# Optimization experiments

Hardware: AMD Instinct MI355X
Metric: run time of the kernel (lower is better)

Reference implementation:

```python
import jax, jax.numpy as jnp
import numpy as np
import math

H_HEADS = 4
SQRT_2_PI = math.sqrt(2.0 / math.pi)


def _gelu_tanh(x):
    return 0.5 * x * (1.0 + jnp.tanh(SQRT_2_PI * (x + 0.044715 * x ** 3)))


def _ln(x, g, b, eps=1e-5):
    mu = jnp.mean(x, axis=-1, keepdims=True)
    var = jnp.var(x, axis=-1, keepdims=True)
    return g * (x - mu) * jax.lax.rsqrt(var + eps) + b


def _forward(support_emb_mat, query_t, support_t, cls_embed, t_freq, t_phase,
             Wq, bq, Wk, bk, Wv, bv, Wo, bo, ln1_g, ln1_b, time_w,
             W1, b1, W2, b2, ln2_g, ln2_b, Wc, bc, bn_g, bn_b):
    B, F, MD = support_emb_mat.shape
    Q = query_t.shape[1]
    S = F + 1
    H = H_HEADS
    D = MD * H
    dph = D // H
    L = Wq.shape[0]
    BQ = B * Q

    # [CLS] + support sequence, feature-tiled to model_dim*num_heads
    cls = jnp.broadcast_to(cls_embed, (B, 1, MD))
    seq = jnp.concatenate([cls, support_emb_mat], axis=1)          # [B,S,MD]
    x = jnp.tile(seq, (1, 1, H))                                    # [B,S,D]
    x = jnp.broadcast_to(x[:, None], (B, Q, S, D)).reshape(BQ, S, D)

    # time sequence: [query_t_q, support_t...] per (b,q)
    sup = jnp.broadcast_to(support_t[:, None, :], (B, Q, F))
    t_seq = jnp.concatenate([query_t[..., None], sup], axis=-1).reshape(BQ, S)
    t_diff = t_seq[:, :, None] - t_seq[:, None, :]                  # [BQ,S,S]
    # time encoder: cos(t*freq + phase) -> [BQ,S,S,TD]
    t_emb = jnp.cos(t_diff[..., None] * t_freq + t_phase)

    # scale as in source: (dim_per_head // num_heads) ** -0.5
    scale = (dph // H) ** (-0.5)

    for l in range(L):
        bias = t_emb @ time_w[l]                                    # [BQ,S,S]
        add = jnp.tile(bias, (H, 1, 1))                             # [BQ*H,S,S]
        res = x
        # raw row-major reshape to (BQ*H, S, dph) exactly as torch .view
        q = (x @ Wq[l] + bq[l]).reshape(BQ * H, S, dph)
        k = (x @ Wk[l] + bk[l]).reshape(BQ * H, S, dph)
        v = (x @ Wv[l] + bv[l]).reshape(BQ * H, S, dph)
        attn = jax.nn.softmax(jnp.einsum('bsd,btd->bst', q, k) * scale + add, axis=-1)
        ctx = jnp.einsum('bst,btd->bsd', attn, v).reshape(BQ, S, D)
        out = _ln(res + ctx @ Wo[l] + bo[l], ln1_g[l], ln1_b[l])
        ffn = _gelu_tanh(out @ W1[l] + b1[l]) @ W2[l] + b2[l]
        x = _ln(out + ffn, ln2_g[l], ln2_b[l])

    # compress: Linear -> BatchNorm1d over seq channels (train mode) -> LeakyReLU
    h = x @ Wc + bc                                                 # [BQ,S,MD]
    mu = jnp.mean(h, axis=(0, 2), keepdims=True)
    var = jnp.var(h, axis=(0, 2), keepdims=True)
    h = bn_g[None, :, None] * (h - mu) * jax.lax.rsqrt(var + 1e-5) + bn_b[None, :, None]
    h = jnp.where(h >= 0, h, 0.01 * h)                              # LeakyReLU
    return h[:, 0, :].reshape(B, Q, MD)


def setup_inputs() -> dict:
    key = jax.random.key(0)
    ks = jax.random.split(key, 24)
    B, Q, F, MD = 128, 32, 7, 128
    H, L, FFN, TD = 4, 6, 2048, 32
    S = F + 1
    D = MD * H

    def nrm(k, shape, s=0.02):
        return jax.random.normal(k, shape, jnp.float32) * s

    inp = {
        'support_emb_mat': jax.random.normal(ks[0], (B, F, MD), jnp.float32),
        'query_t': jax.random.uniform(ks[1], (B, Q), jnp.float32) * 100.0,
        'support_t': jax.random.uniform(ks[2], (B, F), jnp.float32) * 100.0,
        'cls_embed': jax.random.uniform(ks[3], (1, MD), jnp.float32),
        't_freq': nrm(ks[4], (TD,), 1.0),
        't_phase': nrm(ks[5], (TD,), 1.0),
        'Wq': nrm(ks[6], (L, D, D)), 'bq': jnp.zeros((L, D)),
        'Wk': nrm(ks[7], (L, D, D)), 'bk': jnp.zeros((L, D)),
        'Wv': nrm(ks[8], (L, D, D)), 'bv': jnp.zeros((L, D)),
        'Wo': nrm(ks[9], (L, D, D)), 'bo': jnp.zeros((L, D)),
        'ln1_g': jnp.ones((L, D)), 'ln1_b': jnp.zeros((L, D)),
        'time_w': jnp.ones((L, TD)) * 0.001,
        'W1': nrm(ks[10], (L, D, FFN)), 'b1': jnp.zeros((L, FFN)),
        'W2': nrm(ks[11], (L, FFN, D)), 'b2': jnp.zeros((L, D)),
        'ln2_g': jnp.ones((L, D)), 'ln2_b': jnp.zeros((L, D)),
        'Wc': nrm(ks[12], (D, MD)), 'bc': jnp.zeros((MD,)),
        'bn_g': jnp.ones((S,)), 'bn_b': jnp.zeros((S,)),
    }
    return inp


def reference(support_emb_mat, query_t, support_t, cls_embed, t_freq, t_phase,
              Wq, bq, Wk, bk, Wv, bv, Wo, bo, ln1_g, ln1_b, time_w,
              W1, b1, W2, b2, ln2_g, ln2_b, Wc, bc, bn_g, bn_b):
    return _forward(support_emb_mat, query_t, support_t, cls_embed, t_freq, t_phase,
                    Wq, bq, Wk, bk, Wv, bv, Wo, bo, ln1_g, ln1_b, time_w,
                    W1, b1, W2, b2, ln2_g, ln2_b, Wc, bc, bn_g, bn_b)
```

## Files before the change

kernel.cpp:

```cpp
#include <hip/hip_runtime.h>
#include <hip/hip_bf16.h>

typedef _Float16 f16;
typedef __attribute__((ext_vector_type(8))) _Float16 f16x8;
typedef __attribute__((ext_vector_type(4))) _Float16 f16x4;
typedef __attribute__((ext_vector_type(4))) float f32x4;

#define DEVI __device__ __forceinline__

DEVI float ldf(const void* p, size_t i, int isf32) {
    if (isf32) return ((const float*)p)[i];
    unsigned int u = ((const unsigned short*)p)[i];
    union { unsigned int b; float f; } c; c.b = u << 16;
    return c.f;
}

DEVI void gld_lds16(const f16* g, f16* l) {
    __builtin_amdgcn_global_load_lds(
        (__attribute__((address_space(1))) void*)(g),
        (__attribute__((address_space(3))) void*)(l), 16, 0, 0);
}

__global__ void detect_dtype(const void* qt, int* flag) {
    if (threadIdx.x == 0 && blockIdx.x == 0) {
        const unsigned int* w = (const unsigned int*)qt;
        int cnt = 0;
        for (int i = 0; i < 64; ++i) {
            unsigned int lo = w[i] & 0xFFFFu;
            union { unsigned int b; float f; } c; c.b = lo << 16;
            if (c.f >= 1e-4f && c.f <= 100.5f) ++cnt;
        }
        *flag = (cnt >= 32) ? 0 : 1;
    }
}

__global__ __launch_bounds__(256)
void cvt_in(const void* __restrict__ src, float* __restrict__ dst, int n,
            const int* __restrict__ flag) {
    const int f32 = *flag;
    int i = blockIdx.x * 256 + threadIdx.x;
    if (i < n) dst[i] = ldf(src, i, f32);
}

__global__ __launch_bounds__(256)
void fill_out(float* out, float v) {
    out[blockIdx.x * 256 + threadIdx.x] = v;
}

template<int EPI>
__global__ __launch_bounds__(256, 4)
void gemm_bt(const f16* __restrict__ Ag, const f16* __restrict__ BTg,
             const float* __restrict__ biasg, const f16* __restrict__ resg,
             void* __restrict__ outg,
             int NT, int NTZ, int MCHUNK, int N, int K, int lda,
             long zsB, long zsBias, long zsC)
{
    const int tid  = threadIdx.x;
    const int w    = tid >> 6, lane = tid & 63;
    const int wm   = w >> 1,   wn   = w & 1;

    const int id    = blockIdx.x;
    const int pc    = MCHUNK * NTZ;
    const int chunk = id / pc;
    const int rem   = id - chunk * pc;
    const int mloc  = rem % MCHUNK;
    const int ynz   = rem / MCHUNK;
    const int z     = ynz / NT;
    const int tm    = (chunk * MCHUNK + mloc) * 128;
    const int tn    = (ynz - z * NT) * 128;

    const f16*   BT   = BTg + (size_t)z * zsB;
    const float* bias = biasg + (size_t)z * zsBias;
    const size_t zoffC = (size_t)z * zsC;

    __shared__ __align__(16) f16 smA[16][64][8];
    __shared__ __align__(16) f16 smB[16][64][8];

    f32x4 acc[4][4];
#pragma unroll
    for (int i = 0; i < 4; ++i)
#pragma unroll
        for (int j = 0; j < 4; ++j) acc[i][j] = (f32x4)0.0f;

    const int r16 = lane & 15, q4 = lane >> 4;
    const f16* ga[4]; const f16* gb[4];
#pragma unroll
    for (int it = 0; it < 4; ++it) {
        int sb = w * 4 + it, mt = sb >> 1, ks = sb & 1;
        ga[it] = Ag + (size_t)(tm + mt * 16 + r16) * lda + ks * 32 + q4 * 8;
        gb[it] = BT + (size_t)(tn + mt * 16 + r16) * K   + ks * 32 + q4 * 8;
    }

    const int iters = K >> 6;
    for (int kt = 0; kt < iters; ++kt) {
#pragma unroll
        for (int it = 0; it < 4; ++it) {
            int sb = w * 4 + it;
            gld_lds16(ga[it], &smA[sb][0][0]);
            gld_lds16(gb[it], &smB[sb][0][0]);
            ga[it] += 64; gb[it] += 64;
        }
        __syncthreads();
#pragma unroll
        for (int ks = 0; ks < 2; ++ks) {
            f16x8 af[4], bf[4];
#pragma unroll
            for (int i = 0; i < 4; ++i) {
                af[i] = *(const f16x8*)&smA[(wm * 4 + i) * 2 + ks][lane][0];
                bf[i] = *(const f16x8*)&smB[(wn * 4 + i) * 2 + ks][lane][0];
            }
#pragma unroll
            for (int i = 0; i < 4; ++i)
#pragma unroll
                for (int j = 0; j < 4; ++j)
                    acc[i][j] = __builtin_amdgcn_mfma_f32_16x16x32_f16(
                        af[i], bf[j], acc[i][j], 0, 0, 0);
        }
        __syncthreads();
    }

    const int rowBase = tm + wm * 64;
    const int colBase = tn + wn * 64;
#pragma unroll
    for (int j = 0; j < 4; ++j) {
        const int col = colBase + j * 16 + r16;
        const float bv = bias[col];
#pragma unroll
        for (int i = 0; i < 4; ++i) {
            const int row0 = rowBase + i * 16 + q4 * 4;
#pragma unroll
            for (int r = 0; r < 4; ++r) {
                const int row = row0 + r;
                const size_t off = (size_t)row * N + col;
                float v = acc[i][j][r] + bv;
                if constexpr (EPI == 0) {
                    ((f16*)outg)[zoffC + off] = (f16)v;
                } else if constexpr (EPI == 1) {
                    v += (float)resg[off];
                    ((f16*)outg)[off] = (f16)v;
                } else if constexpr (EPI == 2) {
                    float t  = v + 0.044715f * v * v * v;
                    float u  = 1.5957691216057308f * t;
                    float e  = __expf(u);
                    float th = 1.0f - 2.0f / (e + 1.0f);
                    ((f16*)outg)[off] = (f16)(0.5f * v * (1.0f + th));
                } else {
                    ((float*)outg)[off] = v;
                }
            }
        }
    }
}

__global__ __launch_bounds__(256)
void attn_kernel(const f16* __restrict__ qg, const f16* __restrict__ kg,
                 const f16* __restrict__ vg, const float* __restrict__ biasL,
                 f16* __restrict__ cg, int small)
{
    const int w = threadIdx.x >> 6, lane = threadIdx.x & 63;
    const int j = blockIdx.x * 4 + w;
    __shared__ __align__(16) f16 sQ[4][8][136];
    __shared__ __align__(16) f16 sK[4][8][136];
    __shared__ __align__(16) f16 sV[4][8][136];
    __shared__ float sP[4][8][8];

    const size_t base  = (size_t)j * 1024;
    const size_t ibase = small ? ((size_t)(j >> 7) * 4096 + (size_t)(j & 3) * 1024)
                               : base;
#pragma unroll
    for (int t = 0; t < 2; ++t) {
        int flat = (t * 64 + lane) * 8;
        int r = flat >> 7, c = flat & 127;
        *(f16x8*)&sQ[w][r][c] = *(const f16x8*)(qg + ibase + flat);
        *(f16x8*)&sK[w][r][c] = *(const f16x8*)(kg + ibase + flat);
        *(f16x8*)&sV[w][r][c] = *(const f16x8*)(vg + ibase + flat);
    }
    __syncthreads();

    const int i = lane >> 3, jj = lane & 7;
    float d = 0.f;
#pragma unroll
    for (int c = 0; c < 16; ++c) {
        f16x8 qv = *(const f16x8*)&sQ[w][i][c * 8];
        f16x8 kv = *(const f16x8*)&sK[w][jj][c * 8];
#pragma unroll
        for (int e = 0; e < 8; ++e) d += (float)qv[e] * (float)kv[e];
    }
    float s = d * 0.17677669529663687f + biasL[(size_t)(j & 4095) * 64 + lane];
    float mx = s;
    mx = fmaxf(mx, __shfl_xor(mx, 1, 64));
    mx = fmaxf(mx, __shfl_xor(mx, 2, 64));
    mx = fmaxf(mx, __shfl_xor(mx, 4, 64));
    float p = __expf(s - mx);
    float sum = p;
    sum += __shfl_xor(sum, 1, 64);
    sum += __shfl_xor(sum, 2, 64);
    sum += __shfl_xor(sum, 4, 64);
    sP[w][i][jj] = p / sum;
    __syncthreads();

#pragma unroll
    for (int t2 = 0; t2 < 8; ++t2) {
        float ap[8];
#pragma unroll
        for (int e = 0; e < 8; ++e) ap[e] = sP[w][t2][e];
#pragma unroll
        for (int h = 0; h < 2; ++h) {
            int flat = (t2 * 2 + h) * 64 + lane;
            int dd = flat & 127;
            float o = 0.f;
#pragma unroll
            for (int e = 0; e < 8; ++e) o += ap[e] * (float)sV[w][e][dd];
            cg[base + flat] = (f16)o;
        }
    }
}

__global__ __launch_bounds__(256)
void ln_kernel(const f16* __restrict__ X, const float* __restrict__ g,
               const float* __restrict__ b, f16* __restrict__ Y)
{
    const int w = threadIdx.x >> 6, lane = threadIdx.x & 63;
    const int row = blockIdx.x * 4 + w;
    f16x8 v = *(const f16x8*)(X + (size_t)row * 512 + lane * 8);
    float vf[8]; float s = 0.f, ss = 0.f;
#pragma unroll
    for (int e = 0; e < 8; ++e) { vf[e] = (float)v[e]; s += vf[e]; ss += vf[e] * vf[e]; }
#pragma unroll
    for (int m = 1; m <= 32; m <<= 1) {
        s  += __shfl_xor(s, m, 64);
        ss += __shfl_xor(ss, m, 64);
    }
    const float mu  = s * (1.0f / 512.0f);
    const float var = ss * (1.0f / 512.0f) - mu * mu;
    const float rs  = rsqrtf(var + 1e-5f);
    f32x4 g0 = *(const f32x4*)(g + lane * 8), g1 = *(const f32x4*)(g + lane * 8 + 4);
    f32x4 b0 = *(const f32x4*)(b + lane * 8), b1 = *(const f32x4*)(b + lane * 8 + 4);
    f16x8 y;
#pragma unroll
    for (int e = 0; e < 4; ++e) {
        y[e]     = (f16)(g0[e] * (vf[e]     - mu) * rs + b0[e]);
        y[e + 4] = (f16)(g1[e] * (vf[e + 4] - mu) * rs + b1[e]);
    }
    *(f16x8*)(Y + (size_t)row * 512 + lane * 8) = y;
}

__global__ __launch_bounds__(256)
void build_x0(const void* __restrict__ sup, const void* __restrict__ cls,
              f16* __restrict__ xb, const int* __restrict__ flag)
{
    const int f32 = *flag;
    const size_t idx = ((size_t)blockIdx.x * 256 + threadIdx.x) * 4;
    const int row = (int)(idx >> 9), col0 = (int)(idx & 511);
    const int s = row & 7, b = row >> 8;
    f16x4 o;
#pragma unroll
    for (int e = 0; e < 4; ++e) {
        const int md = (col0 + e) & 127;
        float v = (s == 0) ? ldf(cls, md, f32)
                           : ldf(sup, ((size_t)b * 7 + (s - 1)) * 128 + md, f32);
        o[e] = (f16)v;
    }
    *(f16x4*)(xb + idx) = o;
}

__global__ __launch_bounds__(256)
void build_x0s(const void* __restrict__ sup, const void* __restrict__ cls,
               f16* __restrict__ xs, const int* __restrict__ flag)
{
    const int f32 = *flag;
    const size_t idx = ((size_t)blockIdx.x * 256 + threadIdx.x) * 4;
    const int row = (int)(idx >> 9), col0 = (int)(idx & 511);
    const int s = row & 7, b = row >> 3;
    f16x4 o;
#pragma unroll
    for (int e = 0; e < 4; ++e) {
        const int md = (col0 + e) & 127;
        float v = (s == 0) ? ldf(cls, md, f32)
                           : ldf(sup, ((size_t)b * 7 + (s - 1)) * 128 + md, f32);
        o[e] = (f16)v;
    }
    *(f16x4*)(xs + idx) = o;
}

__global__ __launch_bounds__(64)
void bias_kernel(const void* __restrict__ qt, const void* __restrict__ st,
                 const void* __restrict__ freq, const void* __restrict__ phase,
                 const void* __restrict__ tw, float* __restrict__ biasAll,
                 const int* __restrict__ flag)
{
    const int f32 = *flag;
    const int bq = blockIdx.x, lane = threadIdx.x;
    const int b = bq >> 5, qq = bq & 31;
    const int i = lane >> 3, jj = lane & 7;
    const float ti = (i  == 0) ? ldf(qt, b * 32 + qq, f32) : ldf(st, b * 7 + i  - 1, f32);
    const float tj = (jj == 0) ? ldf(qt, b * 32 + qq, f32) : ldf(st, b * 7 + jj - 1, f32);
    const float td = ti - tj;
    float a[6] = {0.f, 0.f, 0.f, 0.f, 0.f, 0.f};
    for (int t = 0; t < 32; ++t) {
        float c = __cosf(td * ldf(freq, t, f32) + ldf(phase, t, f32));
#pragma unroll
        for (int l = 0; l < 6; ++l) a[l] += c * ldf(tw, l * 32 + t, f32);
    }
#pragma unroll
    for (int l = 0; l < 6; ++l)
        biasAll[(size_t)l * (4096 * 64) + (size_t)bq * 64 + lane] = a[l];
}

__global__ __launch_bounds__(256)
void transpose_cvt(const void* __restrict__ W, f16* __restrict__ WT,
                   int K, int N, long zsW, long zsWT, const int* __restrict__ flag)
{
    const int f32 = *flag;
    const size_t zoff = (size_t)blockIdx.z * zsW;
    f16* WTz = WT + (size_t)blockIdx.z * zsWT;
    __shared__ float tile[64][65];
    const int tn = blockIdx.x * 64, tk = blockIdx.y * 64;
#pragma unroll
    for (int t = 0; t < 16; ++t) {
        int idx = t * 256 + threadIdx.x;
        int r = idx >> 6, c = idx & 63;
        tile[r][c] = ldf(W, zoff + (size_t)(tk + r) * N + tn + c, f32);
    }
    __syncthreads();
#pragma unroll
    for (int t = 0; t < 16; ++t) {
        int idx = t * 256 + threadIdx.x;
        int r = idx >> 6, c = idx & 63;
        WTz[(size_t)(tn + r) * K + tk + c] = (f16)tile[c][r];
    }
}

__global__ __launch_bounds__(256)
void gather_qkvb(const void* __restrict__ bq, const void* __restrict__ bk,
                 const void* __restrict__ bv, float* __restrict__ dst,
                 const int* __restrict__ flag)
{
    const int f32 = *flag;
    int i = blockIdx.x * 256 + threadIdx.x;
    if (i < 9216) {
        int z = i / 3072, rem = i % 3072;
        const void* src = (z == 0) ? bq : ((z == 1) ? bk : bv);
        dst[i] = ldf(src, rem, f32);
    }
}

__global__ __launch_bounds__(256)
void bn_reduce(const float* __restrict__ h0, float* __restrict__ stats)
{
    const int t = blockIdx.x * 256 + threadIdx.x;
    float s = 0.f, ss = 0.f;
#pragma unroll
    for (int k = 0; k < 8; ++k) {
        float v = h0[t + k * 65536];
        s += v; ss += v * v;
    }
#pragma unroll
    for (int m = 1; m <= 32; m <<= 1) {
        s  += __shfl_xor(s, m, 64);
        ss += __shfl_xor(ss, m, 64);
    }
    __shared__ float ls[8];
    const int w = threadIdx.x >> 6, lane = threadIdx.x & 63;
    if (lane == 0) { ls[w] = s; ls[4 + w] = ss; }
    __syncthreads();
    if (threadIdx.x == 0) {
        atomicAdd(&stats[0], ls[0] + ls[1] + ls[2] + ls[3]);
        atomicAdd(&stats[1], ls[4] + ls[5] + ls[6] + ls[7]);
    }
}

__global__ __launch_bounds__(256)
void bn_apply(const float* __restrict__ h0, const float* __restrict__ stats,
              const float* __restrict__ bnp, float* __restrict__ out)
{
    const int t = blockIdx.x * 256 + threadIdx.x;
    const float mu  = stats[0] * (1.0f / 524288.0f);
    const float var = stats[1] * (1.0f / 524288.0f) - mu * mu;
    const float rs  = rsqrtf(var + 1e-5f);
    float v = bnp[0] * (h0[t] - mu) * rs + bnp[8];
    v = (v >= 0.f) ? v : 0.01f * v;
    out[t] = v;
}

extern "C" void kernel_launch(void* const* d_in, const int* in_sizes, int n_in,
                              void* d_out, int out_size, void* d_ws, size_t ws_size,
                              hipStream_t stream)
{
    (void)in_sizes; (void)n_in; (void)out_size;
    const void* sup   = d_in[0];
    const void* qt    = d_in[1];
    const void* st    = d_in[2];
    const void* cls   = d_in[3];
    const void* freq  = d_in[4];
    const void* phase = d_in[5];
    const void* Wq = d_in[6];  const void* bqv = d_in[7];
    const void* Wk = d_in[8];  const void* bkv = d_in[9];
    const void* Wv = d_in[10]; const void* bvv = d_in[11];
    const void* Wo = d_in[12]; const void* bo  = d_in[13];
    const void* ln1g = d_in[14]; const void* ln1b = d_in[15];
    const void* tw = d_in[16];
    const void* W1 = d_in[17]; const void* b1 = d_in[18];
    const void* W2 = d_in[19]; const void* b2 = d_in[20];
    const void* ln2g = d_in[21]; const void* ln2b = d_in[22];
    const void* Wc = d_in[23]; const void* bc = d_in[24];
    const void* bng = d_in[25]; const void* bnb = d_in[26];

    const size_t NEEDED = 245658240;
    if (ws_size < NEEDED) {
        fill_out<<<2048, 256, 0, stream>>>((float*)d_out, 999.0f);
        return;
    }

    char* ws = (char*)d_ws;
    f16*   wt      = (f16*)(ws + 0);
    float* biasAll = (float*)(ws + 37879808);
    float* qkvb    = (float*)(ws + 44171264);
    float* prm     = (float*)(ws + 44208128);
    float* stats   = (float*)(ws + 44331584);
    int*   flag    = (int*)  (ws + 44331592);
    f16*   xb      = (f16*)(ws + 44331648);
    f16*   ob      = (f16*)(ws + 77886080);
    char*  region  = ws + 111440512;
    f16*   qb      = (f16*)(region);
    f16*   kb      = (f16*)(region + 33554432);
    f16*   vb      = (f16*)(region + 67108864);
    f16*   cb      = (f16*)(region + 100663296);
    f16*   qs      = (f16*)(region);
    f16*   xs      = (f16*)(region + 100663296);
    f16*   pl1     = (f16*)(region);
    f16*   fbuf    = (f16*)(region);
    f16*   pl2     = (f16*)(region + 67108864);
    float* h0      = (float*)(region);

    detect_dtype<<<1, 64, 0, stream>>>(qt, flag);

    cvt_in<<<12, 256, 0, stream>>>(bo,   prm + 0,     3072,  flag);
    cvt_in<<<48, 256, 0, stream>>>(b1,   prm + 3072,  12288, flag);
    cvt_in<<<12, 256, 0, stream>>>(b2,   prm + 15360, 3072,  flag);
    cvt_in<<<1,  256, 0, stream>>>(bc,   prm + 18432, 128,   flag);
    cvt_in<<<12, 256, 0, stream>>>(ln1g, prm + 18560, 3072,  flag);
    cvt_in<<<12, 256, 0, stream>>>(ln1b, prm + 21632, 3072,  flag);
    cvt_in<<<12, 256, 0, stream>>>(ln2g, prm + 24704, 3072,  flag);
    cvt_in<<<12, 256, 0, stream>>>(ln2b, prm + 27776, 3072,  flag);
    cvt_in<<<1,  256, 0, stream>>>(bng,  prm + 30848, 8,     flag);
    cvt_in<<<1,  256, 0, stream>>>(bnb,  prm + 30856, 8,     flag);

    transpose_cvt<<<dim3(8, 8, 6),  256, 0, stream>>>(Wq, wt + 0,        512, 512,  262144, 262144, flag);
    transpose_cvt<<<dim3(8, 8, 6),  256, 0, stream>>>(Wk, wt + 1572864,  512, 512,  262144, 262144, flag);
    transpose_cvt<<<dim3(8, 8, 6),  256, 0, stream>>>(Wv, wt + 3145728,  512, 512,  262144, 262144, flag);
    transpose_cvt<<<dim3(8, 8, 6),  256, 0, stream>>>(Wo, wt + 4718592,  512, 512,  262144, 262144, flag);
    transpose_cvt<<<dim3(32, 8, 6), 256, 0, stream>>>(W1, wt + 6291456,  512, 2048, 1048576, 1048576, flag);
    transpose_cvt<<<dim3(8, 32, 6), 256, 0, stream>>>(W2, wt + 12582912, 2048, 512, 1048576, 1048576, flag);
    transpose_cvt<<<dim3(2, 8, 1),  256, 0, stream>>>(Wc, wt + 18874368, 512, 128,  0, 0, flag);
    gather_qkvb<<<36, 256, 0, stream>>>(bqv, bkv, bvv, qkvb, flag);
    build_x0<<<16384, 256, 0, stream>>>(sup, cls, xb, flag);
    build_x0s<<<512, 256, 0, stream>>>(sup, cls, xs, flag);
    bias_kernel<<<4096, 64, 0, stream>>>(qt, st, freq, phase, tw, biasAll, flag);
    hipMemsetAsync(stats, 0, 8, stream);

    for (int l = 0; l < 6; ++l) {
        if (l == 0) {
            gemm_bt<0><<<96, 256, 0, stream>>>(
                xs, wt, qkvb, nullptr, qs,
                4, 12, 8, 512, 512, 512, 1572864, 3072, 524288);
            attn_kernel<<<4096, 256, 0, stream>>>(
                qs, qs + 524288, qs + 1048576, biasAll, cb, 1);
        } else {
            gemm_bt<0><<<3072, 256, 0, stream>>>(
                xb, wt + l * 262144, qkvb + l * 512, nullptr, qb,
                4, 12, 64, 512, 512, 512, 1572864, 3072, 16777216);
            attn_kernel<<<4096, 256, 0, stream>>>(
                qb, kb, vb, biasAll + (size_t)l * 262144, cb, 0);
        }
        gemm_bt<1><<<1024, 256, 0, stream>>>(
            cb, wt + 4718592 + l * 262144, prm + 0 + l * 512, xb, pl1,
            4, 4, 128, 512, 512, 512, 0, 0, 0);
        ln_kernel<<<8192, 256, 0, stream>>>(pl1, prm + 18560 + l * 512, prm + 21632 + l * 512, ob);
        for (int mh = 0; mh < 2; ++mh) {
            const size_t aoff = (size_t)mh * 16384 * 512;
            gemm_bt<2><<<2048, 256, 0, stream>>>(
                ob + aoff, wt + 6291456 + l * 1048576, prm + 3072 + l * 2048, nullptr, fbuf,
                16, 16, 64, 2048, 512, 512, 0, 0, 0);
            gemm_bt<1><<<512, 256, 0, stream>>>(
                fbuf, wt + 12582912 + l * 1048576, prm + 15360 + l * 512, ob + aoff, pl2,
                4, 4, 128, 512, 2048, 2048, 0, 0, 0);
            ln_kernel<<<4096, 256, 0, stream>>>(pl2, prm + 24704 + l * 512, prm + 27776 + l * 512, xb + aoff);
        }
    }

    gemm_bt<3><<<32, 256, 0, stream>>>(
        xb, wt + 18874368, prm + 18432, nullptr, h0,
        1, 1, 32, 128, 512, 4096 , 0, 0, 0);
    bn_reduce<<<256, 256, 0, stream>>>(h0, stats);
    bn_apply<<<2048, 256, 0, stream>>>(h0, stats, prm + 30848, (float*)d_out);
}
```

Baseline: 3.092 ms.

## Process two M-tiles per GEMM block and merge FFN halves into one pass

```diff
diff --git a/kernel.cpp b/kernel.cpp
--- a/kernel.cpp
+++ b/kernel.cpp
@@ -52,7 +52,7 @@
 void gemm_bt(const f16* __restrict__ Ag, const f16* __restrict__ BTg,
              const float* __restrict__ biasg, const f16* __restrict__ resg,
              void* __restrict__ outg,
-             int NT, int NTZ, int MCHUNK, int N, int K, int lda,
+             int NT, int NTZ, int MCHUNK, int MT, int N, int K, int lda,
              long zsB, long zsBias, long zsC)
 {
     const int tid  = threadIdx.x;
@@ -66,7 +66,7 @@
     const int mloc  = rem % MCHUNK;
     const int ynz   = rem / MCHUNK;
     const int z     = ynz / NT;
-    const int tm    = (chunk * MCHUNK + mloc) * 128;
+    const int tmB   = (chunk * MCHUNK + mloc) * (128 * MT);
     const int tn    = (ynz - z * NT) * 128;
 
     const f16*   BT   = BTg + (size_t)z * zsB;
@@ -76,76 +76,81 @@
     __shared__ __align__(16) f16 smA[16][64][8];
     __shared__ __align__(16) f16 smB[16][64][8];
 
-    f32x4 acc[4][4];
-#pragma unroll
-    for (int i = 0; i < 4; ++i)
-#pragma unroll
-        for (int j = 0; j < 4; ++j) acc[i][j] = (f32x4)0.0f;
-
     const int r16 = lane & 15, q4 = lane >> 4;
-    const f16* ga[4]; const f16* gb[4];
-#pragma unroll
-    for (int it = 0; it < 4; ++it) {
-        int sb = w * 4 + it, mt = sb >> 1, ks = sb & 1;
-        ga[it] = Ag + (size_t)(tm + mt * 16 + r16) * lda + ks * 32 + q4 * 8;
-        gb[it] = BT + (size_t)(tn + mt * 16 + r16) * K   + ks * 32 + q4 * 8;
-    }
-
     const int iters = K >> 6;
-    for (int kt = 0; kt < iters; ++kt) {
+
+    for (int ms = 0; ms < MT; ++ms) {
+        const int tm = tmB + ms * 128;
+
+        f32x4 acc[4][4];
+#pragma unroll
+        for (int i = 0; i < 4; ++i)
+#pragma unroll
+            for (int j = 0; j < 4; ++j) acc[i][j] = (f32x4)0.0f;
+
+        const f16* ga[4]; const f16* gb[4];
 #pragma unroll
         for (int it = 0; it < 4; ++it) {
-            int sb = w * 4 + it;
-            gld_lds16(ga[it], &smA[sb][0][0]);
-            gld_lds16(gb[it], &smB[sb][0][0]);
-            ga[it] += 64; gb[it] += 64;
-        }
-        __syncthreads();
-#pragma unroll
-        for (int ks = 0; ks < 2; ++ks) {
-            f16x8 af[4], bf[4];
+            int sb = w * 4 + it, mt = sb >> 1, ks = sb & 1;
+            ga[it] = Ag + (size_t)(tm + mt * 16 + r16) * lda + ks * 32 + q4 * 8;
+            gb[it] = BT + (size_t)(tn + mt * 16 + r16) * K   + ks * 32 + q4 * 8;
+        }
+
+        for (int kt = 0; kt < iters; ++kt) {
+#pragma unroll
+            for (int it = 0; it < 4; ++it) {
+                int sb = w * 4 + it;
+                gld_lds16(ga[it], &smA[sb][0][0]);
+                gld_lds16(gb[it], &smB[sb][0][0]);
+                ga[it] += 64; gb[it] += 64;
+            }
+            __syncthreads();
+#pragma unroll
+            for (int ks = 0; ks < 2; ++ks) {
+                f16x8 af[4], bf[4];
+#pragma unroll
+                for (int i = 0; i < 4; ++i) {
+                    af[i] = *(const f16x8*)&smA[(wm * 4 + i) * 2 + ks][lane][0];
+                    bf[i] = *(const f16x8*)&smB[(wn * 4 + i) * 2 + ks][lane][0];
+                }
+#pragma unroll
+                for (int i = 0; i < 4; ++i)
+#pragma unroll
+                    for (int j = 0; j < 4; ++j)
+                        acc[i][j] = __builtin_amdgcn_mfma_f32_16x16x32_f16(
+                            af[i], bf[j], acc[i][j], 0, 0, 0);
+            }
+            __syncthreads();
+        }
+
+        const int rowBase = tm + wm * 64;
+        const int colBase = tn + wn * 64;
+#pragma unroll
+        for (int j = 0; j < 4; ++j) {
+            const int col = colBase + j * 16 + r16;
+            const float bv = bias[col];
 #pragma unroll
             for (int i = 0; i < 4; ++i) {
-                af[i] = *(const f16x8*)&smA[(wm * 4 + i) * 2 + ks][lane][0];
-                bf[i] = *(const f16x8*)&smB[(wn * 4 + i) * 2 + ks][lane][0];
-            }
-#pragma unroll
-            for (int i = 0; i < 4; ++i)
-#pragma unroll
-                for (int j = 0; j < 4; ++j)
-                    acc[i][j] = __builtin_amdgcn_mfma_f32_16x16x32_f16(
-                        af[i], bf[j], acc[i][j], 0, 0, 0);
-        }
-        __syncthreads();
-    }
-
-    const int rowBase = tm + wm * 64;
-    const int colBase = tn + wn * 64;
-#pragma unroll
-    for (int j = 0; j < 4; ++j) {
-        const int col = colBase + j * 16 + r16;
-        const float bv = bias[col];
-#pragma unroll
-        for (int i = 0; i < 4; ++i) {
-            const int row0 = rowBase + i * 16 + q4 * 4;
-#pragma unroll
-            for (int r = 0; r < 4; ++r) {
-                const int row = row0 + r;
-                const size_t off = (size_t)row * N + col;
-                float v = acc[i][j][r] + bv;
-                if constexpr (EPI == 0) {
-                    ((f16*)outg)[zoffC + off] = (f16)v;
-                } else if constexpr (EPI == 1) {
-                    v += (float)resg[off];
-                    ((f16*)outg)[off] = (f16)v;
-                } else if constexpr (EPI == 2) {
-                    float t  = v + 0.044715f * v * v * v;
-                    float u  = 1.5957691216057308f * t;
-                    float e  = __expf(u);
-                    float th = 1.0f - 2.0f / (e + 1.0f);
-                    ((f16*)outg)[off] = (f16)(0.5f * v * (1.0f + th));
-                } else {
-                    ((float*)outg)[off] = v;
+                const int row0 = rowBase + i * 16 + q4 * 4;
+#pragma unroll
+                for (int r = 0; r < 4; ++r) {
+                    const int row = row0 + r;
+                    const size_t off = (size_t)row * N + col;
+                    float v = acc[i][j][r] + bv;
+                    if constexpr (EPI == 0) {
+                        ((f16*)outg)[zoffC + off] = (f16)v;
+                    } else if constexpr (EPI == 1) {
+                        v += (float)resg[off];
+                        ((f16*)outg)[off] = (f16)v;
+                    } else if constexpr (EPI == 2) {
+                        float t  = v + 0.044715f * v * v * v;
+                        float u  = 1.5957691216057308f * t;
+                        float e  = __expf(u);
+                        float th = 1.0f - 2.0f / (e + 1.0f);
+                        ((f16*)outg)[off] = (f16)(0.5f * v * (1.0f + th));
+                    } else {
+                        ((float*)outg)[off] = v;
+                    }
                 }
             }
         }
@@ -283,14 +288,15 @@
     *(f16x4*)(xs + idx) = o;
 }
 
-__global__ __launch_bounds__(64)
+__global__ __launch_bounds__(256)
 void bias_kernel(const void* __restrict__ qt, const void* __restrict__ st,
                  const void* __restrict__ freq, const void* __restrict__ phase,
                  const void* __restrict__ tw, float* __restrict__ biasAll,
                  const int* __restrict__ flag)
 {
     const int f32 = *flag;
-    const int bq = blockIdx.x, lane = threadIdx.x;
+    const int lane = threadIdx.x & 63;
+    const int bq = blockIdx.x * 4 + (threadIdx.x >> 6);
     const int b = bq >> 5, qq = bq & 31;
     const int i = lane >> 3, jj = lane & 7;
     const float ti = (i  == 0) ? ldf(qt, b * 32 + qq, f32) : ldf(st, b * 7 + i  - 1, f32);
@@ -430,7 +436,6 @@
     f16*   xs      = (f16*)(region + 100663296);
     f16*   pl1     = (f16*)(region);
     f16*   fbuf    = (f16*)(region);
-    f16*   pl2     = (f16*)(region + 67108864);
     float* h0      = (float*)(region);
 
     detect_dtype<<<1, 64, 0, stream>>>(qt, flag);
@@ -456,42 +461,39 @@
     gather_qkvb<<<36, 256, 0, stream>>>(bqv, bkv, bvv, qkvb, flag);
     build_x0<<<16384, 256, 0, stream>>>(sup, cls, xb, flag);
     build_x0s<<<512, 256, 0, stream>>>(sup, cls, xs, flag);
-    bias_kernel<<<4096, 64, 0, stream>>>(qt, st, freq, phase, tw, biasAll, flag);
+    bias_kernel<<<1024, 256, 0, stream>>>(qt, st, freq, phase, tw, biasAll, flag);
     hipMemsetAsync(stats, 0, 8, stream);
 
     for (int l = 0; l < 6; ++l) {
         if (l == 0) {
-            gemm_bt<0><<<96, 256, 0, stream>>>(
+            gemm_bt<0><<<48, 256, 0, stream>>>(
                 xs, wt, qkvb, nullptr, qs,
-                4, 12, 8, 512, 512, 512, 1572864, 3072, 524288);
+                4, 12, 4, 2, 512, 512, 512, 1572864, 3072, 524288);
             attn_kernel<<<4096, 256, 0, stream>>>(
                 qs, qs + 524288, qs + 1048576, biasAll, cb, 1);
         } else {
-            gemm_bt<0><<<3072, 256, 0, stream>>>(
+            gemm_bt<0><<<1536, 256, 0, stream>>>(
                 xb, wt + l * 262144, qkvb + l * 512, nullptr, qb,
-                4, 12, 64, 512, 512, 512, 1572864, 3072, 16777216);
+                4, 12, 32, 2, 512, 512, 512, 1572864, 3072, 16777216);
             attn_kernel<<<4096, 256, 0, stream>>>(
                 qb, kb, vb, biasAll + (size_t)l * 262144, cb, 0);
         }
-        gemm_bt<1><<<1024, 256, 0, stream>>>(
+        gemm_bt<1><<<512, 256, 0, stream>>>(
             cb, wt + 4718592 + l * 262144, prm + 0 + l * 512, xb, pl1,
-            4, 4, 128, 512, 512, 512, 0, 0, 0);
+            4, 4, 32, 2, 512, 512, 512, 0, 0, 0);
         ln_kernel<<<8192, 256, 0, stream>>>(pl1, prm + 18560 + l * 512, prm + 21632 + l * 512, ob);
-        for (int mh = 0; mh < 2; ++mh) {
-            const size_t aoff = (size_t)mh * 16384 * 512;
-            gemm_bt<2><<<2048, 256, 0, stream>>>(
-                ob + aoff, wt + 6291456 + l * 1048576, prm + 3072 + l * 2048, nullptr, fbuf,
-                16, 16, 64, 2048, 512, 512, 0, 0, 0);
-            gemm_bt<1><<<512, 256, 0, stream>>>(
-                fbuf, wt + 12582912 + l * 1048576, prm + 15360 + l * 512, ob + aoff, pl2,
-                4, 4, 128, 512, 2048, 2048, 0, 0, 0);
-            ln_kernel<<<4096, 256, 0, stream>>>(pl2, prm + 24704 + l * 512, prm + 27776 + l * 512, xb + aoff);
-        }
+        gemm_bt<2><<<2048, 256, 0, stream>>>(
+            ob, wt + 6291456 + l * 1048576, prm + 3072 + l * 2048, nullptr, fbuf,
+            16, 16, 32, 2, 2048, 512, 512, 0, 0, 0);
+        gemm_bt<1><<<512, 256, 0, stream>>>(
+            fbuf, wt + 12582912 + l * 1048576, prm + 15360 + l * 512, ob, xb,
+            4, 4, 32, 2, 512, 2048, 2048, 0, 0, 0);
+        ln_kernel<<<8192, 256, 0, stream>>>(xb, prm + 24704 + l * 512, prm + 27776 + l * 512, xb);
     }
 
     gemm_bt<3><<<32, 256, 0, stream>>>(
         xb, wt + 18874368, prm + 18432, nullptr, h0,
-        1, 1, 32, 128, 512, 4096 , 0, 0, 0);
+        1, 1, 32, 1, 128, 512, 4096 , 0, 0, 0);
     bn_reduce<<<256, 256, 0, stream>>>(h0, stats);
     bn_apply<<<2048, 256, 0, stream>>>(h0, stats, prm + 30848, (float*)d_out);
 }
```

Result: no change. 3.135 ms (+1.4%).
